# Optimization experiments

Measured on AMD Instinct MI355X. Metric: run time of the kernel, lower is better.

The kernel has to match this reference:

```python
import jax, jax.numpy as jnp
import numpy as np

SEQ, BATCH, HID = 4096, 32, 512

def setup_inputs() -> dict:
    key = jax.random.key(0)
    k1, k2, k3, k4 = jax.random.split(key, 4)
    stdv = 1.0 / np.sqrt(HID)
    x = jax.random.normal(k1, (SEQ, BATCH, HID), dtype=jnp.float32)
    W = jax.random.uniform(k2, (HID, HID), dtype=jnp.float32, minval=-stdv, maxval=stdv)
    b = jax.random.uniform(k3, (HID,), dtype=jnp.float32, minval=-stdv, maxval=stdv)
    context = jax.random.uniform(k4, (HID,), dtype=jnp.float32, minval=-stdv, maxval=stdv)
    return {"x": x, "W": W, "b": b, "context": context}

def reference(x, W, b, context):
    # x: [seq, batch, hid] -> [batch, seq, hid]
    xb = jnp.transpose(x, (1, 0, 2))
    # tanh(Linear(x)) per timestep, batched as one GEMM
    attends = jnp.tanh(jnp.einsum('bsh,oh->bso', xb, W) + b)
    # additive-attention scores via dot with context vector -> [batch, seq]
    similarity = jnp.einsum('bsh,h->bs', attends, context)
    probs = jax.nn.softmax(similarity, axis=-1)  # softmax over seq
    # weighted-sum pooling -> [batch, hid]
    attended = jnp.einsum('bsh,bs->bh', xb, probs)
    return attended
```

## Files before the change

kernel.cpp:

```cpp
#include <hip/hip_runtime.h>
#include <hip/hip_bf16.h>

#define SEQ   4096
#define BATCH 32
#define HID   512
#define MTOT  (SEQ * BATCH)

typedef float  f32x4  __attribute__((ext_vector_type(4)));
typedef __bf16 bf16x8 __attribute__((ext_vector_type(8)));
typedef unsigned short ushort8v __attribute__((ext_vector_type(8)));

__device__ __forceinline__ unsigned short f2bf(float f) {
    unsigned int u = __builtin_bit_cast(unsigned int, f);
    u = (u + 0x7fffu + ((u >> 16) & 1u)) >> 16;
    return (unsigned short)u;
}

__device__ __forceinline__ float tanh_fast(float x) {
    float ax = fabsf(x);
    float e  = __expf(-2.0f * ax);
    float t  = (1.0f - e) * __builtin_amdgcn_rcpf(1.0f + e);
    return copysignf(t, x);
}

__global__ __launch_bounds__(256) void cvt_w_kernel(const float* __restrict__ W,
                                                    unsigned short* __restrict__ Wb) {
    int i = (blockIdx.x * 256 + threadIdx.x) * 4;
    float4 f = *(const float4*)(W + i);
    ushort4 u;
    u.x = f2bf(f.x); u.y = f2bf(f.y); u.z = f2bf(f.z); u.w = f2bf(f.w);
    *(ushort4*)(Wb + i) = u;
}

#define BM 128
#define BN 128
#define BK 64
#define LDSP 72

__global__ __launch_bounds__(256) void gemm_sim_kernel(
    const float* __restrict__ x, const unsigned short* __restrict__ Wb,
    const float* __restrict__ bias, const float* __restrict__ ctx,
    float* __restrict__ sims)
{
    __shared__ unsigned short As[BM][LDSP];
    __shared__ unsigned short Bs[BN][LDSP];

    const int nt = blockIdx.x;
    const int mt = blockIdx.y;
    const int tid  = threadIdx.x;
    const int lane = tid & 63;
    const int wave = tid >> 6;
    const int wm = wave >> 1, wn = wave & 1;
    const int l15 = lane & 15, q = lane >> 4;

    const int rbase = tid >> 3;
    const int kc    = (tid & 7) * 8;

    f32x4 acc[4][4] = {};

    for (int kt = 0; kt < HID / BK; ++kt) {
        const int k0 = kt * BK;
        #pragma unroll
        for (int j = 0; j < 4; ++j) {
            const int row = rbase + j * 32;
            const float4* asrc =
                (const float4*)(x + (size_t)(mt * BM + row) * HID + k0 + kc);
            float4 a0 = asrc[0];
            float4 a1 = asrc[1];
            uint4 bsrc = *(const uint4*)(Wb + (size_t)(nt * BN + row) * HID + k0 + kc);
            ushort8v v;
            v[0] = f2bf(a0.x); v[1] = f2bf(a0.y); v[2] = f2bf(a0.z); v[3] = f2bf(a0.w);
            v[4] = f2bf(a1.x); v[5] = f2bf(a1.y); v[6] = f2bf(a1.z); v[7] = f2bf(a1.w);
            *(ushort8v*)&As[row][kc] = v;
            *(uint4*)&Bs[row][kc]    = bsrc;
        }
        __syncthreads();
        #pragma unroll
        for (int kh = 0; kh < 2; ++kh) {
            bf16x8 af[4], bf[4];
            #pragma unroll
            for (int mi = 0; mi < 4; ++mi)
                af[mi] = *(const bf16x8*)&As[wm * 64 + mi * 16 + l15][kh * 32 + q * 8];
            #pragma unroll
            for (int ni = 0; ni < 4; ++ni)
                bf[ni] = *(const bf16x8*)&Bs[wn * 64 + ni * 16 + l15][kh * 32 + q * 8];
            #pragma unroll
            for (int mi = 0; mi < 4; ++mi)
                #pragma unroll
                for (int ni = 0; ni < 4; ++ni)
                    acc[mi][ni] = __builtin_amdgcn_mfma_f32_16x16x32_bf16(
                        af[mi], bf[ni], acc[mi][ni], 0, 0, 0);
        }
        __syncthreads();
    }

    float ps[16];
    #pragma unroll
    for (int mi = 0; mi < 4; ++mi)
        #pragma unroll
        for (int r = 0; r < 4; ++r) {
            float s = 0.f;
            #pragma unroll
            for (int ni = 0; ni < 4; ++ni) {
                const int o = nt * BN + wn * 64 + ni * 16 + l15;
                float y = acc[mi][ni][r] + bias[o];
                s += ctx[o] * tanh_fast(y);
            }
            ps[mi * 4 + r] = s;
        }
    #pragma unroll
    for (int off = 1; off < 16; off <<= 1)
        #pragma unroll
        for (int i = 0; i < 16; ++i)
            ps[i] += __shfl_xor(ps[i], off, 64);
    if (l15 == 0) {
        #pragma unroll
        for (int mi = 0; mi < 4; ++mi)
            #pragma unroll
            for (int r = 0; r < 4; ++r) {
                const int m = mt * BM + wm * 64 + mi * 16 + q * 4 + r;
                atomicAdd(&sims[m], ps[mi * 4 + r]);
            }
    }
}

__global__ __launch_bounds__(256) void softmax_kernel(const float* __restrict__ sims,
                                                      float* __restrict__ probs) {
    const int b = blockIdx.x;
    const int tid = threadIdx.x;
    const int lane = tid & 63, wave = tid >> 6;
    __shared__ float red[4];

    float v[16];
    #pragma unroll
    for (int i = 0; i < 16; ++i) v[i] = sims[(size_t)(i * 256 + tid) * BATCH + b];

    float mx = -INFINITY;
    #pragma unroll
    for (int i = 0; i < 16; ++i) mx = fmaxf(mx, v[i]);
    #pragma unroll
    for (int off = 32; off >= 1; off >>= 1) mx = fmaxf(mx, __shfl_xor(mx, off, 64));
    if (lane == 0) red[wave] = mx;
    __syncthreads();
    mx = fmaxf(fmaxf(red[0], red[1]), fmaxf(red[2], red[3]));
    __syncthreads();

    float sum = 0.f;
    #pragma unroll
    for (int i = 0; i < 16; ++i) { v[i] = __expf(v[i] - mx); sum += v[i]; }
    #pragma unroll
    for (int off = 32; off >= 1; off >>= 1) sum += __shfl_xor(sum, off, 64);
    if (lane == 0) red[wave] = sum;
    __syncthreads();
    const float inv = 1.0f / (red[0] + red[1] + red[2] + red[3]);

    #pragma unroll
    for (int i = 0; i < 16; ++i)
        probs[(size_t)(i * 256 + tid) * BATCH + b] = v[i] * inv;
}

__global__ __launch_bounds__(512) void attend_kernel(const float* __restrict__ x,
                                                     const float* __restrict__ probs,
                                                     float* __restrict__ out) {
    const int st = blockIdx.x;
    const int b  = blockIdx.y;
    const int h  = threadIdx.x;
    __shared__ float p[128];
    if (h < 128) p[h] = probs[(size_t)(st * 128 + h) * BATCH + b];
    __syncthreads();
    float acc = 0.f;
    const float* xp = x + ((size_t)(st * 128) * BATCH + b) * HID + h;
    #pragma unroll 4
    for (int s = 0; s < 128; ++s)
        acc += p[s] * xp[(size_t)s * BATCH * HID];
    atomicAdd(&out[b * HID + h], acc);
}

extern "C" void kernel_launch(void* const* d_in, const int* in_sizes, int n_in,
                              void* d_out, int out_size, void* d_ws, size_t ws_size,
                              hipStream_t stream) {
    const float* x    = (const float*)d_in[0];
    const float* W    = (const float*)d_in[1];
    const float* bias = (const float*)d_in[2];
    const float* ctx  = (const float*)d_in[3];
    float* out = (float*)d_out;

    unsigned short* Wb = (unsigned short*)d_ws;
    float* sims  = (float*)((char*)d_ws + (512 << 10));
    float* probs = (float*)((char*)d_ws + (1024 << 10));

    hipMemsetAsync(sims, 0, MTOT * sizeof(float), stream);
    hipMemsetAsync(d_out, 0, (size_t)out_size * sizeof(float), stream);

    cvt_w_kernel<<<256, 256, 0, stream>>>(W, Wb);
    gemm_sim_kernel<<<dim3(4, 1024), 256, 0, stream>>>(x, Wb, bias, ctx, sims);
    softmax_kernel<<<32, 256, 0, stream>>>(sims, probs);
    attend_kernel<<<dim3(32, 32), 512, 0, stream>>>(x, probs, out);
}
```

Before: 484.6 us.

## Pre-convert x to bf16, use direct global-to-LDS loads, drop sim atomics

```diff
diff --git a/kernel.cpp b/kernel.cpp
--- a/kernel.cpp
+++ b/kernel.cpp
@@ -9,6 +9,7 @@
 typedef float  f32x4  __attribute__((ext_vector_type(4)));
 typedef __bf16 bf16x8 __attribute__((ext_vector_type(8)));
 typedef unsigned short ushort8v __attribute__((ext_vector_type(8)));
+typedef unsigned int u32;
 
 __device__ __forceinline__ unsigned short f2bf(float f) {
     unsigned int u = __builtin_bit_cast(unsigned int, f);
@@ -21,6 +22,12 @@
     float e  = __expf(-2.0f * ax);
     float t  = (1.0f - e) * __builtin_amdgcn_rcpf(1.0f + e);
     return copysignf(t, x);
+}
+
+__device__ __forceinline__ void g2l16(const void* g, void* l) {
+    __builtin_amdgcn_global_load_lds(
+        (const __attribute__((address_space(1))) u32*)g,
+        (__attribute__((address_space(3))) u32*)l, 16, 0, 0);
 }
 
 __global__ __launch_bounds__(256) void cvt_w_kernel(const float* __restrict__ W,
@@ -32,42 +39,142 @@
     *(ushort4*)(Wb + i) = u;
 }
 
-#define BM 128
-#define BN 128
-#define BK 64
-#define LDSP 72
-
-__global__ __launch_bounds__(256) void gemm_sim_kernel(
-    const float* __restrict__ x, const unsigned short* __restrict__ Wb,
+__global__ __launch_bounds__(256) void cvt_x_kernel(const float* __restrict__ x,
+                                                    unsigned short* __restrict__ xb) {
+    size_t i = ((size_t)blockIdx.x * 256 + threadIdx.x) * 8;
+    float4 a0 = *(const float4*)(x + i);
+    float4 a1 = *(const float4*)(x + i + 4);
+    ushort8v v;
+    v[0] = f2bf(a0.x); v[1] = f2bf(a0.y); v[2] = f2bf(a0.z); v[3] = f2bf(a0.w);
+    v[4] = f2bf(a1.x); v[5] = f2bf(a1.y); v[6] = f2bf(a1.z); v[7] = f2bf(a1.w);
+    *(ushort8v*)(xb + i) = v;
+}
+
+__global__ __launch_bounds__(256) void gemm_sim_bf16(
+    const unsigned short* __restrict__ xb, const unsigned short* __restrict__ Wb,
     const float* __restrict__ bias, const float* __restrict__ ctx,
-    float* __restrict__ sims)
+    float* __restrict__ simsT)
 {
-    __shared__ unsigned short As[BM][LDSP];
-    __shared__ unsigned short Bs[BN][LDSP];
-
-    const int nt = blockIdx.x;
-    const int mt = blockIdx.y;
+    __shared__ __align__(16) unsigned short As[128 * 64];
+    __shared__ __align__(16) unsigned short Bs[128 * 64];
+
+    const int L    = blockIdx.x;
+    const int xcd  = L & 7;
+    const int slot = L >> 3;
+    const int nt   = slot & 3;
+    const int mt   = xcd * 128 + (slot >> 2);
+
     const int tid  = threadIdx.x;
     const int lane = tid & 63;
     const int wave = tid >> 6;
     const int wm = wave >> 1, wn = wave & 1;
     const int l15 = lane & 15, q = lane >> 4;
 
+    const int srow  = lane >> 3;
+    const int skoff = ((lane & 7) ^ srow) * 8;
+
+    const unsigned short* Abase = xb + (size_t)(mt * 128) * HID;
+    const unsigned short* Bbase = Wb + (size_t)(nt * 128) * HID;
+
+    f32x4 acc[4][4] = {};
+
+    for (int kt = 0; kt < HID / 64; ++kt) {
+        const int k0 = kt * 64;
+        #pragma unroll
+        for (int t = 0; t < 4; ++t) {
+            const int c = wave * 4 + t;
+            g2l16(Abase + (size_t)(c * 8 + srow) * HID + k0 + skoff, &As[c * 512]);
+            g2l16(Bbase + (size_t)(c * 8 + srow) * HID + k0 + skoff, &Bs[c * 512]);
+        }
+        __syncthreads();
+        #pragma unroll
+        for (int kh = 0; kh < 2; ++kh) {
+            bf16x8 af[4], bfr[4];
+            const int lc = kh * 4 + q;
+            #pragma unroll
+            for (int mi = 0; mi < 4; ++mi) {
+                const int row = wm * 64 + mi * 16 + l15;
+                af[mi] = *(const bf16x8*)&As[row * 64 + (lc ^ (row & 7)) * 8];
+            }
+            #pragma unroll
+            for (int ni = 0; ni < 4; ++ni) {
+                const int row = wn * 64 + ni * 16 + l15;
+                bfr[ni] = *(const bf16x8*)&Bs[row * 64 + (lc ^ (row & 7)) * 8];
+            }
+            #pragma unroll
+            for (int mi = 0; mi < 4; ++mi)
+                #pragma unroll
+                for (int ni = 0; ni < 4; ++ni)
+                    acc[mi][ni] = __builtin_amdgcn_mfma_f32_16x16x32_bf16(
+                        af[mi], bfr[ni], acc[mi][ni], 0, 0, 0);
+        }
+        __syncthreads();
+    }
+
+    float ps[16];
+    #pragma unroll
+    for (int mi = 0; mi < 4; ++mi)
+        #pragma unroll
+        for (int r = 0; r < 4; ++r) {
+            float s = 0.f;
+            #pragma unroll
+            for (int ni = 0; ni < 4; ++ni) {
+                const int o = nt * 128 + wn * 64 + ni * 16 + l15;
+                float y = acc[mi][ni][r] + bias[o];
+                s += ctx[o] * tanh_fast(y);
+            }
+            ps[mi * 4 + r] = s;
+        }
+    #pragma unroll
+    for (int off = 1; off < 16; off <<= 1)
+        #pragma unroll
+        for (int i = 0; i < 16; ++i)
+            ps[i] += __shfl_xor(ps[i], off, 64);
+    if (l15 == 0) {
+        float* dst = simsT + (size_t)(nt * 2 + wn) * MTOT;
+        #pragma unroll
+        for (int mi = 0; mi < 4; ++mi)
+            #pragma unroll
+            for (int r = 0; r < 4; ++r) {
+                const int m = mt * 128 + wm * 64 + mi * 16 + q * 4 + r;
+                dst[(m & 31) * SEQ + (m >> 5)] = ps[mi * 4 + r];
+            }
+    }
+}
+
+#define LDSP 72
+__global__ __launch_bounds__(256) void gemm_sim_f32(
+    const float* __restrict__ x, const unsigned short* __restrict__ Wb,
+    const float* __restrict__ bias, const float* __restrict__ ctx,
+    float* __restrict__ simsT)
+{
+    __shared__ __align__(16) unsigned short As[128][LDSP];
+    __shared__ __align__(16) unsigned short Bs[128][LDSP];
+
+    const int L    = blockIdx.x;
+    const int xcd  = L & 7;
+    const int slot = L >> 3;
+    const int nt   = slot & 3;
+    const int mt   = xcd * 128 + (slot >> 2);
+
+    const int tid  = threadIdx.x;
+    const int lane = tid & 63;
+    const int wave = tid >> 6;
+    const int wm = wave >> 1, wn = wave & 1;
+    const int l15 = lane & 15, q = lane >> 4;
     const int rbase = tid >> 3;
     const int kc    = (tid & 7) * 8;
 
     f32x4 acc[4][4] = {};
-
-    for (int kt = 0; kt < HID / BK; ++kt) {
-        const int k0 = kt * BK;
+    for (int kt = 0; kt < HID / 64; ++kt) {
+        const int k0 = kt * 64;
         #pragma unroll
         for (int j = 0; j < 4; ++j) {
             const int row = rbase + j * 32;
-            const float4* asrc =
-                (const float4*)(x + (size_t)(mt * BM + row) * HID + k0 + kc);
+            const float4* asrc = (const float4*)(x + (size_t)(mt * 128 + row) * HID + k0 + kc);
             float4 a0 = asrc[0];
             float4 a1 = asrc[1];
-            uint4 bsrc = *(const uint4*)(Wb + (size_t)(nt * BN + row) * HID + k0 + kc);
+            uint4 bsrc = *(const uint4*)(Wb + (size_t)(nt * 128 + row) * HID + k0 + kc);
             ushort8v v;
             v[0] = f2bf(a0.x); v[1] = f2bf(a0.y); v[2] = f2bf(a0.z); v[3] = f2bf(a0.w);
             v[4] = f2bf(a1.x); v[5] = f2bf(a1.y); v[6] = f2bf(a1.z); v[7] = f2bf(a1.w);
@@ -77,23 +184,22 @@
         __syncthreads();
         #pragma unroll
         for (int kh = 0; kh < 2; ++kh) {
-            bf16x8 af[4], bf[4];
+            bf16x8 af[4], bfr[4];
             #pragma unroll
             for (int mi = 0; mi < 4; ++mi)
                 af[mi] = *(const bf16x8*)&As[wm * 64 + mi * 16 + l15][kh * 32 + q * 8];
             #pragma unroll
             for (int ni = 0; ni < 4; ++ni)
-                bf[ni] = *(const bf16x8*)&Bs[wn * 64 + ni * 16 + l15][kh * 32 + q * 8];
+                bfr[ni] = *(const bf16x8*)&Bs[wn * 64 + ni * 16 + l15][kh * 32 + q * 8];
             #pragma unroll
             for (int mi = 0; mi < 4; ++mi)
                 #pragma unroll
                 for (int ni = 0; ni < 4; ++ni)
                     acc[mi][ni] = __builtin_amdgcn_mfma_f32_16x16x32_bf16(
-                        af[mi], bf[ni], acc[mi][ni], 0, 0, 0);
+                        af[mi], bfr[ni], acc[mi][ni], 0, 0, 0);
         }
         __syncthreads();
     }
-
     float ps[16];
     #pragma unroll
     for (int mi = 0; mi < 4; ++mi)
@@ -102,9 +208,8 @@
             float s = 0.f;
             #pragma unroll
             for (int ni = 0; ni < 4; ++ni) {
-                const int o = nt * BN + wn * 64 + ni * 16 + l15;
-                float y = acc[mi][ni][r] + bias[o];
-                s += ctx[o] * tanh_fast(y);
+                const int o = nt * 128 + wn * 64 + ni * 16 + l15;
+                s += ctx[o] * tanh_fast(acc[mi][ni][r] + bias[o]);
             }
             ps[mi * 4 + r] = s;
         }
@@ -114,18 +219,19 @@
         for (int i = 0; i < 16; ++i)
             ps[i] += __shfl_xor(ps[i], off, 64);
     if (l15 == 0) {
+        float* dst = simsT + (size_t)(nt * 2 + wn) * MTOT;
         #pragma unroll
         for (int mi = 0; mi < 4; ++mi)
             #pragma unroll
             for (int r = 0; r < 4; ++r) {
-                const int m = mt * BM + wm * 64 + mi * 16 + q * 4 + r;
-                atomicAdd(&sims[m], ps[mi * 4 + r]);
-            }
-    }
-}
-
-__global__ __launch_bounds__(256) void softmax_kernel(const float* __restrict__ sims,
-                                                      float* __restrict__ probs) {
+                const int m = mt * 128 + wm * 64 + mi * 16 + q * 4 + r;
+                dst[(m & 31) * SEQ + (m >> 5)] = ps[mi * 4 + r];
+            }
+    }
+}
+
+__global__ __launch_bounds__(256) void softmax_kernel(const float* __restrict__ simsT,
+                                                      float* __restrict__ probsT) {
     const int b = blockIdx.x;
     const int tid = threadIdx.x;
     const int lane = tid & 63, wave = tid >> 6;
@@ -133,7 +239,14 @@
 
     float v[16];
     #pragma unroll
-    for (int i = 0; i < 16; ++i) v[i] = sims[(size_t)(i * 256 + tid) * BATCH + b];
+    for (int i = 0; i < 16; ++i) {
+        const int s = i * 256 + tid;
+        float acc = 0.f;
+        #pragma unroll
+        for (int p = 0; p < 8; ++p)
+            acc += simsT[(size_t)p * MTOT + b * SEQ + s];
+        v[i] = acc;
+    }
 
     float mx = -INFINITY;
     #pragma unroll
@@ -156,24 +269,28 @@
 
     #pragma unroll
     for (int i = 0; i < 16; ++i)
-        probs[(size_t)(i * 256 + tid) * BATCH + b] = v[i] * inv;
-}
-
-__global__ __launch_bounds__(512) void attend_kernel(const float* __restrict__ x,
-                                                     const float* __restrict__ probs,
+        probsT[b * SEQ + i * 256 + tid] = v[i] * inv;
+}
+
+__global__ __launch_bounds__(128) void attend_kernel(const float* __restrict__ x,
+                                                     const float* __restrict__ probsT,
                                                      float* __restrict__ out) {
-    const int st = blockIdx.x;
-    const int b  = blockIdx.y;
-    const int h  = threadIdx.x;
+    const int st  = blockIdx.x;
+    const int b   = blockIdx.y;
+    const int tid = threadIdx.x;
     __shared__ float p[128];
-    if (h < 128) p[h] = probs[(size_t)(st * 128 + h) * BATCH + b];
+    p[tid] = probsT[b * SEQ + st * 128 + tid];
     __syncthreads();
-    float acc = 0.f;
-    const float* xp = x + ((size_t)(st * 128) * BATCH + b) * HID + h;
-    #pragma unroll 4
+    f32x4 acc = {};
+    const f32x4* xp = (const f32x4*)x + ((size_t)st * 128 * BATCH + b) * (HID / 4) + tid;
+    #pragma unroll 8
     for (int s = 0; s < 128; ++s)
-        acc += p[s] * xp[(size_t)s * BATCH * HID];
-    atomicAdd(&out[b * HID + h], acc);
+        acc += p[s] * xp[(size_t)s * (BATCH * HID / 4)];
+    float* o = out + b * HID + tid * 4;
+    atomicAdd(o + 0, acc[0]);
+    atomicAdd(o + 1, acc[1]);
+    atomicAdd(o + 2, acc[2]);
+    atomicAdd(o + 3, acc[3]);
 }
 
 extern "C" void kernel_launch(void* const* d_in, const int* in_sizes, int n_in,
@@ -185,15 +302,34 @@
     const float* ctx  = (const float*)d_in[3];
     float* out = (float*)d_out;
 
-    unsigned short* Wb = (unsigned short*)d_ws;
-    float* sims  = (float*)((char*)d_ws + (512 << 10));
-    float* probs = (float*)((char*)d_ws + (1024 << 10));
-
-    hipMemsetAsync(sims, 0, MTOT * sizeof(float), stream);
+    const size_t xb_bytes    = (size_t)MTOT * HID * 2;
+    const size_t wb_bytes    = (size_t)HID * HID * 2;
+    const size_t sims_bytes  = (size_t)8 * MTOT * 4;
+    const size_t probs_bytes = (size_t)MTOT * 4;
+    const bool big = ws_size >= xb_bytes + wb_bytes + sims_bytes + probs_bytes;
+
+    char* w = (char*)d_ws;
+    unsigned short* xb = (unsigned short*)w;
+    unsigned short* Wb;
+    float *simsT, *probsT;
+    if (big) {
+        Wb     = (unsigned short*)(w + xb_bytes);
+        simsT  = (float*)(w + xb_bytes + wb_bytes);
+        probsT = (float*)(w + xb_bytes + wb_bytes + sims_bytes);
+    } else {
+        Wb     = (unsigned short*)w;
+        simsT  = (float*)(w + wb_bytes);
+        probsT = (float*)(w + wb_bytes + sims_bytes);
+    }
+
     hipMemsetAsync(d_out, 0, (size_t)out_size * sizeof(float), stream);
-
-    cvt_w_kernel<<<256, 256, 0, stream>>>(W, Wb);
-    gemm_sim_kernel<<<dim3(4, 1024), 256, 0, stream>>>(x, Wb, bias, ctx, sims);
-    softmax_kernel<<<32, 256, 0, stream>>>(sims, probs);
-    attend_kernel<<<dim3(32, 32), 512, 0, stream>>>(x, probs, out);
-}
+    cvt_w_kernel<<<HID * HID / 1024, 256, 0, stream>>>(W, Wb);
+    if (big) {
+        cvt_x_kernel<<<(int)((size_t)MTOT * HID / 2048), 256, 0, stream>>>(x, xb);
+        gemm_sim_bf16<<<4096, 256, 0, stream>>>(xb, Wb, bias, ctx, simsT);
+    } else {
+        gemm_sim_f32<<<4096, 256, 0, stream>>>(x, Wb, bias, ctx, simsT);
+    }
+    softmax_kernel<<<BATCH, 256, 0, stream>>>(simsT, probsT);
+    attend_kernel<<<dim3(32, 32), 128, 0, stream>>>(x, probsT, out);
+}
```

Result: slower. 557.2 us (+15.0%).
